# Optimization experiments

Hardware: AMD Instinct MI355X
Metric: run time of the kernel (lower is better)

## Reference

```python
import jax, jax.numpy as jnp
import numpy as np

B = 8
DIM = 256          # __init__ dim; input has 2*DIM channels
H = 32
W = 32
NUM_HEADS = 4
DH_QK = 64         # make_divisible(256*1.0, 8) // 4
DH_V = 64          # dim_out // num_heads
DQK = NUM_HEADS * DH_QK   # 256
DV = NUM_HEADS * DH_V     # 256
SCALE = DH_QK ** -0.5
HIDDEN = 4 * DIM          # mlp_ratio=4 applied to dim
DIM_OUT = DIM
EPS = 1e-5


def setup_inputs() -> dict:
    key = jax.random.key(0)
    ks = jax.random.split(key, 8)
    qkv_out = 2 * DQK + DV   # 768
    return {
        "x": jax.random.normal(ks[0], (B, 2 * DIM, H, W), jnp.float32),
        "qkv_f_w": jax.random.normal(ks[1], (qkv_out, DIM), jnp.float32) * DIM ** -0.5,
        "qkv_p_w": jax.random.normal(ks[2], (qkv_out, DIM), jnp.float32) * DIM ** -0.5,
        "height_rel": jax.random.normal(ks[3], (2 * H - 1, DH_QK), jnp.float32) * SCALE,
        "width_rel": jax.random.normal(ks[4], (2 * W - 1, DH_QK), jnp.float32) * SCALE,
        "ln_gamma": jnp.ones((2 * DV, H, W), jnp.float32),
        "ln_beta": jnp.zeros((2 * DV, H, W), jnp.float32),
        "fc1_w": jax.random.normal(ks[5], (HIDDEN, 2 * DV), jnp.float32) * (2 * DV) ** -0.5,
        "fc1_b": jnp.zeros((HIDDEN,), jnp.float32),
        "fc2_w": jax.random.normal(ks[6], (DIM_OUT, HIDDEN), jnp.float32) * HIDDEN ** -0.5,
        "fc2_b": jnp.zeros((DIM_OUT,), jnp.float32),
    }


def _rel_to_abs(x):
    # x: (b, L, 2L-1) -> (b, L, L) via the pad/reshape shift trick
    b, L, _ = x.shape
    x = jnp.pad(x, ((0, 0), (0, 0), (0, 1)))          # (b, L, 2L)
    xf = x.reshape(b, L * 2 * L)
    xf = jnp.pad(xf, ((0, 0), (0, L - 1)))
    return xf.reshape(b, L + 1, 2 * L - 1)[:, :L, L - 1:]


def _rel_logits_1d(q, rel_k, perm):
    # q: (b, h, w, d); rel_k: (2w-1, d) -> (b, h, w, h, w) after perm
    b, h, w, _ = q.shape
    x = jnp.einsum('bhwd,md->bhwm', q, rel_k).reshape(b * h, w, 2 * w - 1)
    x = _rel_to_abs(x).reshape(b, h, 1, w, w)
    x = jnp.broadcast_to(x, (b, h, h, w, w))
    return x.transpose(perm)


def _pos_embed(q, height_rel, width_rel):
    # q: (B*nh, HW, d) -> relative-position logits (B*nh, HW, HW)
    bh = q.shape[0]
    qs = q.reshape(bh, H, W, DH_QK)
    lw = _rel_logits_1d(qs, width_rel, (0, 1, 3, 2, 4))
    lh = _rel_logits_1d(qs.transpose(0, 2, 1, 3), height_rel, (0, 3, 1, 4, 2))
    return (lh + lw).reshape(bh, H * W, H * W)


def _get_qkv(x, w):
    # 1x1 conv as channel GEMM; x: (B, DIM, H, W)
    qkv = jnp.einsum('bchw,oc->bohw', x, w)
    q, k, v = jnp.split(qkv, [DQK, 2 * DQK], axis=1)
    q = q.reshape(B * NUM_HEADS, DH_QK, H * W).transpose(0, 2, 1)  # (Bh, HW, d)
    k = k.reshape(B * NUM_HEADS, DH_QK, H * W)                      # (Bh, d, HW)
    v = v.reshape(B * NUM_HEADS, DH_V, H * W).transpose(0, 2, 1)    # (Bh, HW, d)
    return q, k, v


def _apply_attn(q, k, v, height_rel, width_rel):
    logits = jnp.einsum('bnd,bdm->bnm', q, k) * SCALE + _pos_embed(q, height_rel, width_rel)
    attn = jax.nn.softmax(logits, axis=-1)
    out = jnp.einsum('bnm,bmd->bnd', attn, v)                       # (Bh, HW, dv)
    return out.transpose(0, 2, 1).reshape(B, DV, H, W)


def reference(x, qkv_f_w, qkv_p_w, height_rel, width_rel, ln_gamma, ln_beta,
              fc1_w, fc1_b, fc2_w, fc2_b):
    x1, x2 = x[:, :DIM], x[:, DIM:]
    qf, kf, vf = _get_qkv(x1, qkv_f_w)
    qp, kp, vp = _get_qkv(x2, qkv_p_w)
    out_f = _apply_attn(qf, kp, vp, height_rel, width_rel)
    out_p = _apply_attn(qp, kf, vf, height_rel, width_rel)
    xpf = jnp.concatenate([out_f, out_p], axis=1)                   # (B, 2*DV, H, W)
    # LayerNorm over normalized_shape = [2*DV, H, W]
    mean = xpf.mean(axis=(1, 2, 3), keepdims=True)
    var = jnp.var(xpf, axis=(1, 2, 3), keepdims=True)
    xpf = (xpf - mean) * jax.lax.rsqrt(var + EPS) * ln_gamma + ln_beta
    # conv-MLP (1x1 convs), exact GELU as torch default
    h = jnp.einsum('bchw,oc->bohw', xpf, fc1_w) + fc1_b[None, :, None, None]
    h = jax.nn.gelu(h, approximate=False)
    out = jnp.einsum('bchw,oc->bohw', h, fc2_w) + fc2_b[None, :, None, None]
    return out  # stride=1 -> pool is identity
```

## Files before the change

### kernel.cpp

```cpp
#include <hip/hip_runtime.h>

#define SCALE 0.125f

typedef short short8 __attribute__((ext_vector_type(8)));
typedef float f32x4 __attribute__((ext_vector_type(4)));
typedef unsigned short us8 __attribute__((ext_vector_type(8)));

__device__ __forceinline__ unsigned short f2bf(float x) {
  unsigned int u = __float_as_uint(x);
  u += 0x7fff + ((u >> 16) & 1);
  return (unsigned short)(u >> 16);
}
__device__ __forceinline__ float bf2f(unsigned short b) {
  return __uint_as_float(((unsigned int)b) << 16);
}
__device__ __forceinline__ float gelu_exact(float x) {
  return 0.5f * x * (1.0f + erff(x * 0.70710678118654752f));
}

__global__ __launch_bounds__(256)
void cast_w(const float* __restrict__ qf, const float* __restrict__ qp,
            const float* __restrict__ f1, const float* __restrict__ f2,
            unsigned short* __restrict__ wc)
{
  const int i4 = (blockIdx.x * 256 + threadIdx.x) * 4;
  const float* src; int off;
  if (i4 < 196608)      { src = qf; off = i4; }
  else if (i4 < 393216) { src = qp; off = i4 - 196608; }
  else if (i4 < 917504) { src = f1; off = i4 - 393216; }
  else                  { src = f2; off = i4 - 917504; }
  const float4 v = *(const float4*)(src + off);
  ushort4 o;
  o.x = f2bf(v.x); o.y = f2bf(v.y); o.z = f2bf(v.z); o.w = f2bf(v.w);
  *(ushort4*)(wc + i4) = o;
}

__global__ __launch_bounds__(256)
void trans_x(const float* __restrict__ x, unsigned short* __restrict__ xT)
{
  __shared__ unsigned short L[64 * 72];
  const int ch0 = blockIdx.x * 64, tok0 = blockIdx.y * 64, z = blockIdx.z;
  const int b = z & 7, path = z >> 3;
  const float* src = x + (size_t)b * 524288 + (size_t)(path * 256 + ch0) * 1024 + tok0;
#pragma unroll
  for (int t = 0; t < 4; ++t) {
    const int i = threadIdx.x + t * 256;
    const int row = i >> 4, c4 = (i & 15) * 4;
    const float4 v = *(const float4*)(src + (size_t)row * 1024 + c4);
    L[(c4 + 0) * 72 + row] = f2bf(v.x);
    L[(c4 + 1) * 72 + row] = f2bf(v.y);
    L[(c4 + 2) * 72 + row] = f2bf(v.z);
    L[(c4 + 3) * 72 + row] = f2bf(v.w);
  }
  __syncthreads();
  unsigned short* dst = xT + (size_t)z * 262144 + (size_t)tok0 * 256 + ch0;
#pragma unroll
  for (int t = 0; t < 2; ++t) {
    const int i = threadIdx.x + t * 256;
    const int row = i >> 3, c8 = (i & 7) * 8;
    *(us8*)(dst + (size_t)row * 256 + c8) = *(const us8*)&L[row * 72 + c8];
  }
}

__global__ __launch_bounds__(256)
void trans_gb(const float* __restrict__ gamma, const float* __restrict__ beta,
              unsigned short* __restrict__ gbT)
{
  __shared__ unsigned short L[64 * 72];
  const int ch0 = blockIdx.x * 64, tok0 = blockIdx.y * 64, which = blockIdx.z;
  const float* src = (which ? beta : gamma) + (size_t)ch0 * 1024 + tok0;
#pragma unroll
  for (int t = 0; t < 4; ++t) {
    const int i = threadIdx.x + t * 256;
    const int row = i >> 4, c4 = (i & 15) * 4;
    const float4 v = *(const float4*)(src + (size_t)row * 1024 + c4);
    L[(c4 + 0) * 72 + row] = f2bf(v.x);
    L[(c4 + 1) * 72 + row] = f2bf(v.y);
    L[(c4 + 2) * 72 + row] = f2bf(v.z);
    L[(c4 + 3) * 72 + row] = f2bf(v.w);
  }
  __syncthreads();
  unsigned short* dst = gbT + (size_t)which * 524288 + (size_t)tok0 * 512 + ch0;
#pragma unroll
  for (int t = 0; t < 2; ++t) {
    const int i = threadIdx.x + t * 256;
    const int row = i >> 3, c8 = (i & 7) * 8;
    *(us8*)(dst + (size_t)row * 512 + c8) = *(const us8*)&L[row * 72 + c8];
  }
}

template<int MODE, int K>
__global__ __launch_bounds__(256, 3)
void gemm_mf(const unsigned short* __restrict__ A0, const unsigned short* __restrict__ B0,
             unsigned short* __restrict__ qkT, unsigned short* __restrict__ vb,
             unsigned short* __restrict__ hT, float* __restrict__ outF,
             const float* __restrict__ bias)
{
  __shared__ unsigned short As[2][4096];
  __shared__ unsigned short Bs[2][4096];
  const int tid = threadIdx.x;
  const int lane = tid & 63, w = tid >> 6;
  const int c = lane & 15, g = lane >> 4;
  const int wm = w >> 1, wn = w & 1;
  const int m0 = blockIdx.x * 128, n0 = blockIdx.y * 128;
  const int z = blockIdx.z;

  const unsigned short* A;
  const unsigned short* B;
  if (MODE == 0) {
    A = A0 + (size_t)(z >> 3) * 196608;
    B = B0 + (size_t)z * 262144;
  } else {
    A = A0;
    B = B0 + (size_t)z * 1024 * K;
  }

  f32x4 acc[4][4];
#pragma unroll
  for (int mi = 0; mi < 4; ++mi)
#pragma unroll
    for (int ni = 0; ni < 4; ++ni) acc[mi][ni] = (f32x4){0.f, 0.f, 0.f, 0.f};

  us8 a_r[2], b_r[2];
#pragma unroll
  for (int t = 0; t < 2; ++t) {
    const int i = tid + t * 256;
    const int row = i >> 2, kc = (i & 3) * 8;
    a_r[t] = *(const us8*)(A + (size_t)(m0 + row) * K + kc);
    b_r[t] = *(const us8*)(B + (size_t)(n0 + row) * K + kc);
  }

  int buf = 0;
  const int NK = K / 32;
  for (int ks = 0; ks < NK; ++ks) {
#pragma unroll
    for (int t = 0; t < 2; ++t) {
      const int i = tid + t * 256;
      const int row = i >> 2, kc = i & 3;
      const int p = row * 32 + ((kc ^ (row & 3)) * 8);
      *(us8*)&As[buf][p] = a_r[t];
      *(us8*)&Bs[buf][p] = b_r[t];
    }
    __syncthreads();
    if (ks + 1 < NK) {
      const int k0 = (ks + 1) * 32;
#pragma unroll
      for (int t = 0; t < 2; ++t) {
        const int i = tid + t * 256;
        const int row = i >> 2, kc = (i & 3) * 8;
        a_r[t] = *(const us8*)(A + (size_t)(m0 + row) * K + k0 + kc);
        b_r[t] = *(const us8*)(B + (size_t)(n0 + row) * K + k0 + kc);
      }
    }
    short8 aF[4], bF[4];
#pragma unroll
    for (int mi = 0; mi < 4; ++mi) {
      const int row = 64 * wm + 16 * mi + c;
      aF[mi] = *(const short8*)&As[buf][row * 32 + ((g ^ (row & 3)) * 8)];
    }
#pragma unroll
    for (int ni = 0; ni < 4; ++ni) {
      const int row = 64 * wn + 16 * ni + c;
      bF[ni] = *(const short8*)&Bs[buf][row * 32 + ((g ^ (row & 3)) * 8)];
    }
#pragma unroll
    for (int mi = 0; mi < 4; ++mi)
#pragma unroll
      for (int ni = 0; ni < 4; ++ni)
        acc[mi][ni] = __builtin_amdgcn_mfma_f32_16x16x32_bf16(aF[mi], bF[ni], acc[mi][ni], 0, 0, 0);
    buf ^= 1;
  }

  if (MODE == 0) {
#pragma unroll
    for (int mi = 0; mi < 4; ++mi) {
      const int mb = m0 + 64 * wm + 16 * mi + 4 * g;
#pragma unroll
      for (int ni = 0; ni < 4; ++ni) {
        const int n = n0 + 64 * wn + 16 * ni + c;
        if (mb < 512) {
          ushort4 o4;
          o4.x = f2bf(acc[mi][ni][0]); o4.y = f2bf(acc[mi][ni][1]);
          o4.z = f2bf(acc[mi][ni][2]); o4.w = f2bf(acc[mi][ni][3]);
          *(ushort4*)(qkT + (size_t)z * 524288 + (size_t)n * 512 + mb) = o4;
        } else {
#pragma unroll
          for (int r = 0; r < 4; ++r)
            vb[(size_t)z * 262144 + (size_t)(mb - 512 + r) * 1024 + n] = f2bf(acc[mi][ni][r]);
        }
      }
    }
  } else if (MODE == 1) {
#pragma unroll
    for (int mi = 0; mi < 4; ++mi) {
      const int mb = m0 + 64 * wm + 16 * mi + 4 * g;
      const float4 b4 = *(const float4*)(bias + mb);
#pragma unroll
      for (int ni = 0; ni < 4; ++ni) {
        const int n = n0 + 64 * wn + 16 * ni + c;
        ushort4 o4;
        o4.x = f2bf(gelu_exact(acc[mi][ni][0] + b4.x));
        o4.y = f2bf(gelu_exact(acc[mi][ni][1] + b4.y));
        o4.z = f2bf(gelu_exact(acc[mi][ni][2] + b4.z));
        o4.w = f2bf(gelu_exact(acc[mi][ni][3] + b4.w));
        *(ushort4*)(hT + (size_t)z * 1048576 + (size_t)n * 1024 + mb) = o4;
      }
    }
  } else {
#pragma unroll
    for (int mi = 0; mi < 4; ++mi) {
      const int mb = m0 + 64 * wm + 16 * mi + 4 * g;
      const float4 b4 = *(const float4*)(bias + mb);
#pragma unroll
      for (int ni = 0; ni < 4; ++ni) {
        const int n = n0 + 64 * wn + 16 * ni + c;
        float* op = outF + (size_t)z * 262144 + (size_t)mb * 1024 + n;
        op[0]    = acc[mi][ni][0] + b4.x;
        op[1024] = acc[mi][ni][1] + b4.y;
        op[2048] = acc[mi][ni][2] + b4.z;
        op[3072] = acc[mi][ni][3] + b4.w;
      }
    }
  }
}

__global__ __launch_bounds__(512, 4)
void attn_k(const unsigned short* __restrict__ qkT,
            const unsigned short* __restrict__ vbuf,
            const float* __restrict__ hrel,
            const float* __restrict__ wrel,
            unsigned short* __restrict__ xpfT,
            float* __restrict__ stats)
{
  __shared__ unsigned short lds[25088];
  unsigned short* Ks  = lds;
  unsigned short* Vs  = lds + 4096;
  unsigned short* Ps  = lds + 8192;
  unsigned short* QHb = lds + 16384;
  unsigned short* QWb = lds;

  const int tid = threadIdx.x;
  const int lane = tid & 63, w = tid >> 6;
  const int c = lane & 15, g = lane >> 4;
  const int n0 = blockIdx.x * 128;
  const int bh = blockIdx.y, pOut = blockIdx.z;
  const int b = bh >> 2, head = bh & 3, pKV = 1 - pOut;

  const unsigned short* Qg = qkT + (size_t)(pOut * 8 + b) * 524288 + head * 64;
  const unsigned short* Kg = qkT + (size_t)(pKV * 8 + b) * 524288 + 256 + head * 64;
  const unsigned short* Vg = vbuf + ((size_t)(pKV * 8 + b) * 256 + head * 64) * 1024;

  const int srow = tid >> 3, sc8 = (tid & 7) * 8;
  us8 kr = *(const us8*)(Kg + (size_t)srow * 512 + sc8);
  us8 vr = *(const us8*)(Vg + (size_t)srow * 1024 + sc8);

#pragma unroll
  for (int t = 0; t < 2; ++t) {
    const int i = tid + t * 512;
    const int row = i >> 3, ch = i & 7;
    *(us8*)&Ps[row * 64 + ((ch ^ (row & 7)) * 8)] =
        *(const us8*)(Qg + (size_t)(n0 + row) * 512 + ch * 8);
  }
  for (int i = tid; i < 4032; i += 512) {
    const int r = i >> 6, d = i & 63;
    const int p = r * 64 + (((d >> 3) ^ (r & 7)) * 8) + (d & 7);
    Ks[p] = f2bf(wrel[i]);
    Vs[p] = f2bf(hrel[i]);
  }
  if (tid < 64) {
    const int p = 63 * 64 + (((tid >> 3) ^ 7) * 8) + (tid & 7);
    Ks[p] = 0; Vs[p] = 0;
  }
  __syncthreads();

  const int qrow = 16 * w + c;
  const short8 aQ0 = *(const short8*)&Ps[qrow * 64 + ((g ^ (qrow & 7)) * 8)];
  const short8 aQ1 = *(const short8*)&Ps[qrow * 64 + (((4 + g) ^ (qrow & 7)) * 8)];

  f32x4 qwf[4], qhf[4];
#pragma unroll
  for (int f = 0; f < 4; ++f) {
    const int rr = 16 * f + c;
    const short8 w0 = *(const short8*)&Ks[rr * 64 + ((g ^ (rr & 7)) * 8)];
    const short8 w1 = *(const short8*)&Ks[rr * 64 + (((4 + g) ^ (rr & 7)) * 8)];
    f32x4 z0 = {0.f, 0.f, 0.f, 0.f};
    z0 = __builtin_amdgcn_mfma_f32_16x16x32_bf16(aQ0, w0, z0, 0, 0, 0);
    z0 = __builtin_amdgcn_mfma_f32_16x16x32_bf16(aQ1, w1, z0, 0, 0, 0);
    qwf[f] = z0;
    const short8 h0 = *(const short8*)&Vs[rr * 64 + ((g ^ (rr & 7)) * 8)];
    const short8 h1 = *(const short8*)&Vs[rr * 64 + (((4 + g) ^ (rr & 7)) * 8)];
    f32x4 z1 = {0.f, 0.f, 0.f, 0.f};
    z1 = __builtin_amdgcn_mfma_f32_16x16x32_bf16(aQ0, h0, z1, 0, 0, 0);
    z1 = __builtin_amdgcn_mfma_f32_16x16x32_bf16(aQ1, h1, z1, 0, 0, 0);
    qhf[f] = z1;
  }
  __syncthreads();
#pragma unroll
  for (int f = 0; f < 4; ++f)
#pragma unroll
    for (int r = 0; r < 4; ++r) {
      const int i = 16 * w + 4 * g + r;
      QWb[i * 64 + 16 * f + c] = f2bf(qwf[f][r]);
      QHb[i * 68 + 16 * f + c] = f2bf(qhf[f][r]);
    }
  __syncthreads();

  float qw0[4], qw1[4];
  int qhrow[4];
  float lsum[4] = {0.f, 0.f, 0.f, 0.f};
#pragma unroll
  for (int r = 0; r < 4; ++r) {
    const int i = 16 * w + 4 * g + r;
    const int qa = n0 + i;
    const int w1i = qa & 31, h1 = (qa >> 5) & 31;
    qw0[r] = bf2f(QWb[i * 64 + (c - w1i + 31)]);
    qw1[r] = bf2f(QWb[i * 64 + (c + 16 - w1i + 31)]);
    qhrow[r] = i * 68 + (31 - h1);
  }
  __syncthreads();

  f32x4 O[4];
#pragma unroll
  for (int f = 0; f < 4; ++f) O[f] = (f32x4){0.f, 0.f, 0.f, 0.f};

  const int spos = srow * 64 + (((tid & 7) ^ (srow & 7)) * 8);
  for (int mt = 0; mt < 16; ++mt) {
    *(us8*)&Ks[spos] = kr;
    *(us8*)&Vs[spos] = vr;
    __syncthreads();
    if (mt < 15) {
      const int m0n = (mt + 1) * 64;
      kr = *(const us8*)(Kg + (size_t)(m0n + srow) * 512 + sc8);
      vr = *(const us8*)(Vg + (size_t)srow * 1024 + m0n + sc8);
    }
    f32x4 Sf[4];
#pragma unroll
    for (int f = 0; f < 4; ++f) {
      const int jr = 16 * f + c;
      const short8 b0 = *(const short8*)&Ks[jr * 64 + ((g ^ (jr & 7)) * 8)];
      const short8 b1 = *(const short8*)&Ks[jr * 64 + (((4 + g) ^ (jr & 7)) * 8)];
      f32x4 z = {0.f, 0.f, 0.f, 0.f};
      z = __builtin_amdgcn_mfma_f32_16x16x32_bf16(aQ0, b0, z, 0, 0, 0);
      z = __builtin_amdgcn_mfma_f32_16x16x32_bf16(aQ1, b1, z, 0, 0, 0);
      Sf[f] = z;
    }
    float qhv[4][2];
#pragma unroll
    for (int r = 0; r < 4; ++r) {
      qhv[r][0] = bf2f(QHb[qhrow[r] + 2 * mt]);
      qhv[r][1] = bf2f(QHb[qhrow[r] + 2 * mt + 1]);
    }
#pragma unroll
    for (int f = 0; f < 4; ++f) {
      const int half = f >> 1;
      const float* qwf2 = (f & 1) ? qw1 : qw0;
#pragma unroll
      for (int r = 0; r < 4; ++r) {
        const float p = __expf(fmaf(Sf[f][r], SCALE, qhv[r][half] + qwf2[r]));
        lsum[r] += p;
        const int i = 16 * w + 4 * g + r;
        Ps[i * 64 + (((2 * f + (c >> 3)) ^ (i & 7)) * 8) + (c & 7)] = f2bf(p);
      }
    }
    const short8 aP0 = *(const short8*)&Ps[qrow * 64 + ((g ^ (qrow & 7)) * 8)];
    const short8 aP1 = *(const short8*)&Ps[qrow * 64 + (((4 + g) ^ (qrow & 7)) * 8)];
#pragma unroll
    for (int f = 0; f < 4; ++f) {
      const int dr = 16 * f + c;
      const short8 b0 = *(const short8*)&Vs[dr * 64 + ((g ^ (dr & 7)) * 8)];
      const short8 b1 = *(const short8*)&Vs[dr * 64 + (((4 + g) ^ (dr & 7)) * 8)];
      O[f] = __builtin_amdgcn_mfma_f32_16x16x32_bf16(aP0, b0, O[f], 0, 0, 0);
      O[f] = __builtin_amdgcn_mfma_f32_16x16x32_bf16(aP1, b1, O[f], 0, 0, 0);
    }
    __syncthreads();
  }

#pragma unroll
  for (int off = 1; off < 16; off <<= 1)
#pragma unroll
    for (int r = 0; r < 4; ++r) lsum[r] += __shfl_xor(lsum[r], off);

  float o[4][4];
  float ssum = 0.f, ssq = 0.f;
#pragma unroll
  for (int r = 0; r < 4; ++r) {
    const float linv = 1.0f / lsum[r];
#pragma unroll
    for (int f = 0; f < 4; ++f) {
      const float v = O[f][r] * linv;
      o[f][r] = v;
      ssum += v;
      ssq = fmaf(v, v, ssq);
    }
  }
#pragma unroll
  for (int off = 1; off < 64; off <<= 1) {
    ssum += __shfl_xor(ssum, off);
    ssq  += __shfl_xor(ssq, off);
  }
  if (lane == 0) {
    atomicAdd(&stats[b * 2 + 0], ssum);
    atomicAdd(&stats[b * 2 + 1], ssq);
  }

#pragma unroll
  for (int f = 0; f < 4; ++f)
#pragma unroll
    for (int r = 0; r < 4; ++r) {
      const int i = 16 * w + 4 * g + r;
      Ps[i * 64 + (((2 * f + (c >> 3)) ^ (i & 7)) * 8) + (c & 7)] = f2bf(o[f][r]);
    }
  __syncthreads();
  unsigned short* dst = xpfT + ((size_t)b * 1024 + n0) * 512 + pOut * 256 + head * 64;
#pragma unroll
  for (int t = 0; t < 2; ++t) {
    const int i = tid + t * 512;
    const int row = i >> 3, ch = i & 7;
    *(us8*)(dst + (size_t)row * 512 + ch * 8) = *(const us8*)&Ps[row * 64 + ((ch ^ (row & 7)) * 8)];
  }
}

__global__ __launch_bounds__(256)
void ln_k(const unsigned short* __restrict__ xpfT, const unsigned short* __restrict__ gbT,
          const float* __restrict__ stats, unsigned short* __restrict__ xln)
{
  const int i = blockIdx.x * 256 + threadIdx.x;
  const int b = i >> 16, off = i & 65535;
  const float invN = 1.0f / 524288.0f;
  const float mean = stats[b * 2] * invN;
  const float var = stats[b * 2 + 1] * invN - mean * mean;
  const float rstd = rsqrtf(var + 1e-5f);
  const us8 xv = *(const us8*)(xpfT + (size_t)i * 8);
  const us8 gv = *(const us8*)(gbT + (size_t)off * 8);
  const us8 bv = *(const us8*)(gbT + 524288 + (size_t)off * 8);
  us8 ov;
#pragma unroll
  for (int j = 0; j < 8; ++j)
    ov[j] = f2bf((bf2f(xv[j]) - mean) * rstd * bf2f(gv[j]) + bf2f(bv[j]));
  *(us8*)(xln + (size_t)i * 8) = ov;
}

extern "C" void kernel_launch(void* const* d_in, const int* in_sizes, int n_in,
                              void* d_out, int out_size, void* d_ws, size_t ws_size,
                              hipStream_t stream)
{
  const float* x     = (const float*)d_in[0];
  const float* qkvfw = (const float*)d_in[1];
  const float* qkvpw = (const float*)d_in[2];
  const float* hrel  = (const float*)d_in[3];
  const float* wrel  = (const float*)d_in[4];
  const float* gamma = (const float*)d_in[5];
  const float* beta  = (const float*)d_in[6];
  const float* fc1w  = (const float*)d_in[7];
  const float* fc1b  = (const float*)d_in[8];
  const float* fc2w  = (const float*)d_in[9];
  const float* fc2b  = (const float*)d_in[10];
  float* out = (float*)d_out;

  float* stats = (float*)d_ws;
  unsigned short* wc   = (unsigned short*)(stats + 64);
  unsigned short* xT   = wc + 1179648;
  unsigned short* gbT  = xT + 4194304;
  unsigned short* qkT  = gbT + 1048576;
  unsigned short* vbuf = qkT + 8388608;
  unsigned short* xpfT = vbuf + 4194304;
  unsigned short* hT   = xpfT + 4194304;

  hipMemsetAsync(stats, 0, 64 * sizeof(float), stream);

  cast_w<<<1152, 256, 0, stream>>>(qkvfw, qkvpw, fc1w, fc2w, wc);
  trans_x<<<dim3(4, 16, 16), 256, 0, stream>>>(x, xT);
  trans_gb<<<dim3(8, 16, 2), 256, 0, stream>>>(gamma, beta, gbT);

  gemm_mf<0, 256><<<dim3(6, 8, 16), 256, 0, stream>>>(
      wc, xT, qkT, vbuf, nullptr, nullptr, nullptr);

  attn_k<<<dim3(8, 32, 2), 512, 0, stream>>>(qkT, vbuf, hrel, wrel, xpfT, stats);

  ln_k<<<2048, 256, 0, stream>>>(xpfT, gbT, stats, xT);

  gemm_mf<1, 512><<<dim3(8, 8, 8), 256, 0, stream>>>(
      wc + 393216, xT, nullptr, nullptr, hT, nullptr, fc1b);

  gemm_mf<2, 1024><<<dim3(2, 8, 8), 256, 0, stream>>>(
      wc + 917504, hT, nullptr, nullptr, nullptr, out, fc2b);
}
```

Measured before the change: 292.7 us.

## Load attention K/V fragments directly from global memory, drop LDS staging and barriers

The attention kernel moves from 512-thread blocks covering 128 queries to 256-thread blocks covering 64 queries. Each wave now loads its Q, K and V MFMA operands straight from global memory into registers, and it computes S transposed so the softmax row sum is per-lane. This removes the per-tile LDS staging and the __syncthreads in the inner loop. Relative-position tables are read and cast per wave instead of staged cooperatively. The change trades LDS traffic and block-wide synchronisation for redundant global/L2 loads of K/V across waves and less explicit prefetching.

```diff
diff --git a/kernel.cpp b/kernel.cpp
--- a/kernel.cpp
+++ b/kernel.cpp
@@ -224,7 +224,7 @@
   }
 }
 
-__global__ __launch_bounds__(512, 4)
+__global__ __launch_bounds__(256, 4)
 void attn_k(const unsigned short* __restrict__ qkT,
             const unsigned short* __restrict__ vbuf,
             const float* __restrict__ hrel,
@@ -232,167 +232,139 @@
             unsigned short* __restrict__ xpfT,
             float* __restrict__ stats)
 {
-  __shared__ unsigned short lds[25088];
-  unsigned short* Ks  = lds;
-  unsigned short* Vs  = lds + 4096;
-  unsigned short* Ps  = lds + 8192;
-  unsigned short* QHb = lds + 16384;
+  __shared__ unsigned short lds[64 * 72 + 64 * 68];
+  unsigned short* Ps  = lds;
   unsigned short* QWb = lds;
+  unsigned short* QHb = lds + 64 * 72;
 
   const int tid = threadIdx.x;
   const int lane = tid & 63, w = tid >> 6;
   const int c = lane & 15, g = lane >> 4;
-  const int n0 = blockIdx.x * 128;
-  const int bh = blockIdx.y, pOut = blockIdx.z;
+  const int xb = blockIdx.x;
+  const int pOut = xb >> 5, bh = xb & 31;
   const int b = bh >> 2, head = bh & 3, pKV = 1 - pOut;
+  const int n0 = blockIdx.y * 64;
 
   const unsigned short* Qg = qkT + (size_t)(pOut * 8 + b) * 524288 + head * 64;
   const unsigned short* Kg = qkT + (size_t)(pKV * 8 + b) * 524288 + 256 + head * 64;
   const unsigned short* Vg = vbuf + ((size_t)(pKV * 8 + b) * 256 + head * 64) * 1024;
 
-  const int srow = tid >> 3, sc8 = (tid & 7) * 8;
-  us8 kr = *(const us8*)(Kg + (size_t)srow * 512 + sc8);
-  us8 vr = *(const us8*)(Vg + (size_t)srow * 1024 + sc8);
-
-#pragma unroll
-  for (int t = 0; t < 2; ++t) {
-    const int i = tid + t * 512;
-    const int row = i >> 3, ch = i & 7;
-    *(us8*)&Ps[row * 64 + ((ch ^ (row & 7)) * 8)] =
-        *(const us8*)(Qg + (size_t)(n0 + row) * 512 + ch * 8);
-  }
-  for (int i = tid; i < 4032; i += 512) {
-    const int r = i >> 6, d = i & 63;
-    const int p = r * 64 + (((d >> 3) ^ (r & 7)) * 8) + (d & 7);
-    Ks[p] = f2bf(wrel[i]);
-    Vs[p] = f2bf(hrel[i]);
-  }
-  if (tid < 64) {
-    const int p = 63 * 64 + (((tid >> 3) ^ 7) * 8) + (tid & 7);
-    Ks[p] = 0; Vs[p] = 0;
-  }
-  __syncthreads();
-
-  const int qrow = 16 * w + c;
-  const short8 aQ0 = *(const short8*)&Ps[qrow * 64 + ((g ^ (qrow & 7)) * 8)];
-  const short8 aQ1 = *(const short8*)&Ps[qrow * 64 + (((4 + g) ^ (qrow & 7)) * 8)];
-
-  f32x4 qwf[4], qhf[4];
+  const int qr = 16 * w + c;
+  const short8 aQ0 = *(const short8*)(Qg + (size_t)(n0 + qr) * 512 + 8 * g);
+  const short8 aQ1 = *(const short8*)(Qg + (size_t)(n0 + qr) * 512 + 32 + 8 * g);
+
 #pragma unroll
   for (int f = 0; f < 4; ++f) {
     const int rr = 16 * f + c;
-    const short8 w0 = *(const short8*)&Ks[rr * 64 + ((g ^ (rr & 7)) * 8)];
-    const short8 w1 = *(const short8*)&Ks[rr * 64 + (((4 + g) ^ (rr & 7)) * 8)];
-    f32x4 z0 = {0.f, 0.f, 0.f, 0.f};
-    z0 = __builtin_amdgcn_mfma_f32_16x16x32_bf16(aQ0, w0, z0, 0, 0, 0);
-    z0 = __builtin_amdgcn_mfma_f32_16x16x32_bf16(aQ1, w1, z0, 0, 0, 0);
-    qwf[f] = z0;
-    const short8 h0 = *(const short8*)&Vs[rr * 64 + ((g ^ (rr & 7)) * 8)];
-    const short8 h1 = *(const short8*)&Vs[rr * 64 + (((4 + g) ^ (rr & 7)) * 8)];
-    f32x4 z1 = {0.f, 0.f, 0.f, 0.f};
-    z1 = __builtin_amdgcn_mfma_f32_16x16x32_bf16(aQ0, h0, z1, 0, 0, 0);
-    z1 = __builtin_amdgcn_mfma_f32_16x16x32_bf16(aQ1, h1, z1, 0, 0, 0);
-    qhf[f] = z1;
-  }
+    const int rrc = rr < 63 ? rr : 62;
+    const float sc = rr < 63 ? 1.f : 0.f;
+    const float4 wa = *(const float4*)(wrel + rrc * 64 + 8 * g);
+    const float4 wb = *(const float4*)(wrel + rrc * 64 + 8 * g + 4);
+    const float4 wcv = *(const float4*)(wrel + rrc * 64 + 32 + 8 * g);
+    const float4 wd = *(const float4*)(wrel + rrc * 64 + 32 + 8 * g + 4);
+    const float4 ha = *(const float4*)(hrel + rrc * 64 + 8 * g);
+    const float4 hb = *(const float4*)(hrel + rrc * 64 + 8 * g + 4);
+    const float4 hc = *(const float4*)(hrel + rrc * 64 + 32 + 8 * g);
+    const float4 hd = *(const float4*)(hrel + rrc * 64 + 32 + 8 * g + 4);
+    short8 w0, w1, h0, h1;
+    w0[0]=f2bf(wa.x*sc); w0[1]=f2bf(wa.y*sc); w0[2]=f2bf(wa.z*sc); w0[3]=f2bf(wa.w*sc);
+    w0[4]=f2bf(wb.x*sc); w0[5]=f2bf(wb.y*sc); w0[6]=f2bf(wb.z*sc); w0[7]=f2bf(wb.w*sc);
+    w1[0]=f2bf(wcv.x*sc); w1[1]=f2bf(wcv.y*sc); w1[2]=f2bf(wcv.z*sc); w1[3]=f2bf(wcv.w*sc);
+    w1[4]=f2bf(wd.x*sc); w1[5]=f2bf(wd.y*sc); w1[6]=f2bf(wd.z*sc); w1[7]=f2bf(wd.w*sc);
+    h0[0]=f2bf(ha.x*sc); h0[1]=f2bf(ha.y*sc); h0[2]=f2bf(ha.z*sc); h0[3]=f2bf(ha.w*sc);
+    h0[4]=f2bf(hb.x*sc); h0[5]=f2bf(hb.y*sc); h0[6]=f2bf(hb.z*sc); h0[7]=f2bf(hb.w*sc);
+    h1[0]=f2bf(hc.x*sc); h1[1]=f2bf(hc.y*sc); h1[2]=f2bf(hc.z*sc); h1[3]=f2bf(hc.w*sc);
+    h1[4]=f2bf(hd.x*sc); h1[5]=f2bf(hd.y*sc); h1[6]=f2bf(hd.z*sc); h1[7]=f2bf(hd.w*sc);
+    f32x4 zw = {0.f, 0.f, 0.f, 0.f};
+    zw = __builtin_amdgcn_mfma_f32_16x16x32_bf16(aQ0, w0, zw, 0, 0, 0);
+    zw = __builtin_amdgcn_mfma_f32_16x16x32_bf16(aQ1, w1, zw, 0, 0, 0);
+    f32x4 zh = {0.f, 0.f, 0.f, 0.f};
+    zh = __builtin_amdgcn_mfma_f32_16x16x32_bf16(aQ0, h0, zh, 0, 0, 0);
+    zh = __builtin_amdgcn_mfma_f32_16x16x32_bf16(aQ1, h1, zh, 0, 0, 0);
+#pragma unroll
+    for (int r = 0; r < 4; ++r) {
+      QWb[(16 * w + 4 * g + r) * 68 + 16 * f + c] = f2bf(zw[r]);
+      QHb[(16 * w + 4 * g + r) * 68 + 16 * f + c] = f2bf(zh[r]);
+    }
+  }
+  const int qa = n0 + qr;
+  const int w1i = qa & 31, h1i = qa >> 5;
+  float qwv[2][4];
+#pragma unroll
+  for (int p = 0; p < 2; ++p)
+#pragma unroll
+    for (int r = 0; r < 4; ++r)
+      qwv[p][r] = bf2f(QWb[qr * 68 + 16 * p + 4 * g + r - w1i + 31]);
+  const int qhbase = qr * 68 + 31 - h1i;
   __syncthreads();
-#pragma unroll
-  for (int f = 0; f < 4; ++f)
-#pragma unroll
-    for (int r = 0; r < 4; ++r) {
-      const int i = 16 * w + 4 * g + r;
-      QWb[i * 64 + 16 * f + c] = f2bf(qwf[f][r]);
-      QHb[i * 68 + 16 * f + c] = f2bf(qhf[f][r]);
-    }
-  __syncthreads();
-
-  float qw0[4], qw1[4];
-  int qhrow[4];
-  float lsum[4] = {0.f, 0.f, 0.f, 0.f};
-#pragma unroll
-  for (int r = 0; r < 4; ++r) {
-    const int i = 16 * w + 4 * g + r;
-    const int qa = n0 + i;
-    const int w1i = qa & 31, h1 = (qa >> 5) & 31;
-    qw0[r] = bf2f(QWb[i * 64 + (c - w1i + 31)]);
-    qw1[r] = bf2f(QWb[i * 64 + (c + 16 - w1i + 31)]);
-    qhrow[r] = i * 68 + (31 - h1);
-  }
-  __syncthreads();
-
+
+  float lsum = 0.f;
   f32x4 O[4];
 #pragma unroll
   for (int f = 0; f < 4; ++f) O[f] = (f32x4){0.f, 0.f, 0.f, 0.f};
 
-  const int spos = srow * 64 + (((tid & 7) ^ (srow & 7)) * 8);
+#pragma unroll 2
   for (int mt = 0; mt < 16; ++mt) {
-    *(us8*)&Ks[spos] = kr;
-    *(us8*)&Vs[spos] = vr;
-    __syncthreads();
-    if (mt < 15) {
-      const int m0n = (mt + 1) * 64;
-      kr = *(const us8*)(Kg + (size_t)(m0n + srow) * 512 + sc8);
-      vr = *(const us8*)(Vg + (size_t)srow * 1024 + m0n + sc8);
+    const int m0 = mt * 64;
+    short8 vB[4][2], kA[4][2];
+#pragma unroll
+    for (int f = 0; f < 4; ++f) {
+      const unsigned short* vp = Vg + (size_t)(16 * f + c) * 1024 + m0 + 8 * g;
+      vB[f][0] = *(const short8*)(vp);
+      vB[f][1] = *(const short8*)(vp + 32);
+      const unsigned short* kp = Kg + (size_t)(m0 + 16 * f + c) * 512 + 8 * g;
+      kA[f][0] = *(const short8*)(kp);
+      kA[f][1] = *(const short8*)(kp + 32);
     }
     f32x4 Sf[4];
 #pragma unroll
     for (int f = 0; f < 4; ++f) {
-      const int jr = 16 * f + c;
-      const short8 b0 = *(const short8*)&Ks[jr * 64 + ((g ^ (jr & 7)) * 8)];
-      const short8 b1 = *(const short8*)&Ks[jr * 64 + (((4 + g) ^ (jr & 7)) * 8)];
       f32x4 z = {0.f, 0.f, 0.f, 0.f};
-      z = __builtin_amdgcn_mfma_f32_16x16x32_bf16(aQ0, b0, z, 0, 0, 0);
-      z = __builtin_amdgcn_mfma_f32_16x16x32_bf16(aQ1, b1, z, 0, 0, 0);
+      z = __builtin_amdgcn_mfma_f32_16x16x32_bf16(kA[f][0], aQ0, z, 0, 0, 0);
+      z = __builtin_amdgcn_mfma_f32_16x16x32_bf16(kA[f][1], aQ1, z, 0, 0, 0);
       Sf[f] = z;
     }
-    float qhv[4][2];
-#pragma unroll
-    for (int r = 0; r < 4; ++r) {
-      qhv[r][0] = bf2f(QHb[qhrow[r] + 2 * mt]);
-      qhv[r][1] = bf2f(QHb[qhrow[r] + 2 * mt + 1]);
-    }
+    const float qh0 = bf2f(QHb[qhbase + 2 * mt]);
+    const float qh1 = bf2f(QHb[qhbase + 2 * mt + 1]);
 #pragma unroll
     for (int f = 0; f < 4; ++f) {
-      const int half = f >> 1;
-      const float* qwf2 = (f & 1) ? qw1 : qw0;
-#pragma unroll
-      for (int r = 0; r < 4; ++r) {
-        const float p = __expf(fmaf(Sf[f][r], SCALE, qhv[r][half] + qwf2[r]));
-        lsum[r] += p;
-        const int i = 16 * w + 4 * g + r;
-        Ps[i * 64 + (((2 * f + (c >> 3)) ^ (i & 7)) * 8) + (c & 7)] = f2bf(p);
-      }
-    }
-    const short8 aP0 = *(const short8*)&Ps[qrow * 64 + ((g ^ (qrow & 7)) * 8)];
-    const short8 aP1 = *(const short8*)&Ps[qrow * 64 + (((4 + g) ^ (qrow & 7)) * 8)];
+      const float qh = (f >= 2) ? qh1 : qh0;
+      const float* qwp = qwv[f & 1];
+      float p0 = __expf(fmaf(Sf[f][0], SCALE, qh + qwp[0]));
+      float p1 = __expf(fmaf(Sf[f][1], SCALE, qh + qwp[1]));
+      float p2 = __expf(fmaf(Sf[f][2], SCALE, qh + qwp[2]));
+      float p3 = __expf(fmaf(Sf[f][3], SCALE, qh + qwp[3]));
+      lsum += (p0 + p1) + (p2 + p3);
+      ushort4 pk;
+      pk.x = f2bf(p0); pk.y = f2bf(p1); pk.z = f2bf(p2); pk.w = f2bf(p3);
+      *(ushort4*)&Ps[qr * 72 + 16 * f + 4 * g] = pk;
+    }
+    const short8 aP0 = *(const short8*)&Ps[qr * 72 + 8 * g];
+    const short8 aP1 = *(const short8*)&Ps[qr * 72 + 32 + 8 * g];
 #pragma unroll
     for (int f = 0; f < 4; ++f) {
-      const int dr = 16 * f + c;
-      const short8 b0 = *(const short8*)&Vs[dr * 64 + ((g ^ (dr & 7)) * 8)];
-      const short8 b1 = *(const short8*)&Vs[dr * 64 + (((4 + g) ^ (dr & 7)) * 8)];
-      O[f] = __builtin_amdgcn_mfma_f32_16x16x32_bf16(aP0, b0, O[f], 0, 0, 0);
-      O[f] = __builtin_amdgcn_mfma_f32_16x16x32_bf16(aP1, b1, O[f], 0, 0, 0);
-    }
-    __syncthreads();
-  }
-
-#pragma unroll
-  for (int off = 1; off < 16; off <<= 1)
-#pragma unroll
-    for (int r = 0; r < 4; ++r) lsum[r] += __shfl_xor(lsum[r], off);
+      O[f] = __builtin_amdgcn_mfma_f32_16x16x32_bf16(aP0, vB[f][0], O[f], 0, 0, 0);
+      O[f] = __builtin_amdgcn_mfma_f32_16x16x32_bf16(aP1, vB[f][1], O[f], 0, 0, 0);
+    }
+  }
+
+  lsum += __shfl_xor(lsum, 16);
+  lsum += __shfl_xor(lsum, 32);
+  float linv[4];
+#pragma unroll
+  for (int r = 0; r < 4; ++r) linv[r] = 1.0f / __shfl(lsum, 4 * g + r);
 
   float o[4][4];
   float ssum = 0.f, ssq = 0.f;
 #pragma unroll
-  for (int r = 0; r < 4; ++r) {
-    const float linv = 1.0f / lsum[r];
-#pragma unroll
-    for (int f = 0; f < 4; ++f) {
-      const float v = O[f][r] * linv;
+  for (int f = 0; f < 4; ++f)
+#pragma unroll
+    for (int r = 0; r < 4; ++r) {
+      const float v = O[f][r] * linv[r];
       o[f][r] = v;
       ssum += v;
       ssq = fmaf(v, v, ssq);
     }
-  }
 #pragma unroll
   for (int off = 1; off < 64; off <<= 1) {
     ssum += __shfl_xor(ssum, off);
@@ -406,17 +378,15 @@
 #pragma unroll
   for (int f = 0; f < 4; ++f)
 #pragma unroll
-    for (int r = 0; r < 4; ++r) {
-      const int i = 16 * w + 4 * g + r;
-      Ps[i * 64 + (((2 * f + (c >> 3)) ^ (i & 7)) * 8) + (c & 7)] = f2bf(o[f][r]);
-    }
+    for (int r = 0; r < 4; ++r)
+      Ps[(16 * w + 4 * g + r) * 72 + 16 * f + c] = f2bf(o[f][r]);
   __syncthreads();
   unsigned short* dst = xpfT + ((size_t)b * 1024 + n0) * 512 + pOut * 256 + head * 64;
 #pragma unroll
   for (int t = 0; t < 2; ++t) {
-    const int i = tid + t * 512;
-    const int row = i >> 3, ch = i & 7;
-    *(us8*)(dst + (size_t)row * 512 + ch * 8) = *(const us8*)&Ps[row * 64 + ((ch ^ (row & 7)) * 8)];
+    const int i = tid + t * 256;
+    const int row = i >> 3, c8 = (i & 7) * 8;
+    *(us8*)(dst + (size_t)row * 512 + c8) = *(const us8*)&Ps[row * 72 + c8];
   }
 }
 
@@ -475,7 +445,7 @@
   gemm_mf<0, 256><<<dim3(6, 8, 16), 256, 0, stream>>>(
       wc, xT, qkT, vbuf, nullptr, nullptr, nullptr);
 
-  attn_k<<<dim3(8, 32, 2), 512, 0, stream>>>(qkT, vbuf, hrel, wrel, xpfT, stats);
+  attn_k<<<dim3(64, 16), 256, 0, stream>>>(qkT, vbuf, hrel, wrel, xpfT, stats);
 
   ln_k<<<2048, 256, 0, stream>>>(xpfT, gbT, stats, xT);
 
```

Result: slower. 387.3 us (+32.3%).
